# Optimization experiments

Measured on AMD Instinct MI355X. Metric: run time of the kernel, lower is better.

The kernel has to match this reference:

```python
import jax, jax.numpy as jnp
import numpy as np

# Detect() defaults from the source
NUM_CLASSES = 2
TOP_K = 750          # max detections returned per class
NMS_TOP_K = 5000     # candidates considered by NMS
NMS_THRESH = 0.3
CONF_THRESH = 0.05
VAR0, VAR1 = 0.1, 0.2  # prior box variances


def decode(loc, priors):
    # loc, priors: [P,4]; priors in (cx,cy,w,h); returns corner boxes [P,4]
    xy = priors[:, :2] + loc[:, :2] * VAR0 * priors[:, 2:]
    wh = priors[:, 2:] * jnp.exp(loc[:, 2:] * VAR1)
    x1y1 = xy - wh * 0.5
    x2y2 = x1y1 + wh
    return jnp.concatenate([x1y1, x2y2], axis=1)


def nms_single(boxes, scores):
    # boxes [P,4], scores [P] -> kept rows [TOP_K,5] = (score, x1,y1,x2,y2)
    s = jnp.where(scores > CONF_THRESH, scores, -1.0)
    top_s, top_i = jax.lax.top_k(s, NMS_TOP_K)   # restrict to best nms_top_k candidates
    cb = boxes[top_i]                             # [K,4] candidate boxes
    area = (cb[:, 2] - cb[:, 0]) * (cb[:, 3] - cb[:, 1])
    ar = jnp.arange(NMS_TOP_K)

    def step(s_cur, _):
        i = jnp.argmax(s_cur)                     # highest-scoring unsuppressed box
        sc = s_cur[i]
        ok = sc > 0.0                             # any valid candidate left?
        b = cb[i]
        xx1 = jnp.maximum(cb[:, 0], b[0])
        yy1 = jnp.maximum(cb[:, 1], b[1])
        xx2 = jnp.minimum(cb[:, 2], b[2])
        yy2 = jnp.minimum(cb[:, 3], b[3])
        inter = jnp.clip(xx2 - xx1, 0.0) * jnp.clip(yy2 - yy1, 0.0)
        union = area - inter + area[i]
        iou = inter / union
        supp = (iou > NMS_THRESH) | (ar == i)     # suppress overlapping + self
        s_next = jnp.where(ok & supp, -1.0, s_cur)
        row = jnp.where(ok, jnp.concatenate([sc[None], b]), jnp.zeros(5, boxes.dtype))
        return s_next, row

    _, rows = jax.lax.scan(step, top_s, None, length=TOP_K)
    return rows  # [TOP_K, 5]


def setup_inputs() -> dict:
    key = jax.random.key(0)
    k1, k2, k3 = jax.random.split(key, 3)
    B, P = 8, 136500
    loc_data = jax.random.normal(k1, (B, P, 4), jnp.float32)
    conf_data = jax.random.normal(k2, (B, P, 2), jnp.float32)
    u = jax.random.uniform(k3, (P, 4), jnp.float32)
    # priors: cx,cy in (0,1); w,h small positive (normalized coords)
    prior_data = jnp.concatenate([u[:, :2], u[:, 2:] * 0.1 + 0.01], axis=1)
    return {"loc_data": loc_data, "conf_data": conf_data, "prior_data": prior_data}


def reference(loc_data, conf_data, prior_data):
    B = loc_data.shape[0]
    conf = jax.nn.softmax(conf_data, axis=-1)                    # [B,P,2]
    boxes = jax.vmap(lambda l: decode(l, prior_data))(loc_data)  # [B,P,4]
    rows = jax.vmap(nms_single)(boxes, conf[:, :, 1])            # [B,TOP_K,5]
    out = jnp.zeros((B, NUM_CLASSES, TOP_K, 5), loc_data.dtype)  # class 0 = background, all zeros
    out = out.at[:, 1].set(rows)
    return out
```

## Files before the change

### kernel.cpp

```cpp
#include <hip/hip_runtime.h>
#include <stdint.h>

#pragma clang fp contract(off)

#define NPRI   136500
#define BATCH  8
#define NMS_K  5000
#define NKPAD  5120
#define TOPK   750
#define SORT_N 8192
#define HBINS  1024
#define HOFF   0x3D40
#define MROW   80
#define CNTSTRIDE 32
#define CUT    32

typedef unsigned long long u64;

__device__ __forceinline__ u64 shfl64(u64 v, int src) {
    int lo = __shfl((int)(unsigned)(v & 0xffffffffull), src);
    int hi = __shfl((int)(unsigned)(v >> 32), src);
    return ((u64)(unsigned)hi << 32) | (u64)(unsigned)lo;
}
__device__ __forceinline__ u64 shfl64_xor(u64 v, int m) {
    int lo = __shfl_xor((int)(unsigned)(v & 0xffffffffull), m);
    int hi = __shfl_xor((int)(unsigned)(v >> 32), m);
    return ((u64)(unsigned)hi << 32) | (u64)(unsigned)lo;
}

__device__ __forceinline__ bool iou_sup(float4 c4, float aj,
                                        float4 rbx, float ra) {
    float xx1 = fmaxf(c4.x, rbx.x);
    float yy1 = fmaxf(c4.y, rbx.y);
    float xx2 = fminf(c4.z, rbx.z);
    float yy2 = fminf(c4.w, rbx.w);
    float iw = fmaxf(xx2 - xx1, 0.0f);
    float ih = fmaxf(yy2 - yy1, 0.0f);
    float inter = iw * ih;
    float uni = (aj - inter) + ra;
    float u = fmaf(-0.3f, uni, inter);
    float d = fmaf(-1.4901161193847656e-8f, uni, u);
    return d > 0.0f;
}
__device__ __forceinline__ u64 iou_word(float4 c4, float aj,
                                        float4 rbx, float ra) {
    return __ballot(iou_sup(c4, aj, rbx, ra));
}

__device__ __forceinline__ u64 diag_mask(u64 word, int sh) {
    if (sh >= 0)
        word &= (sh >= 63) ? 0ull : (~0ull << (sh + 1));
    return word;
}

__device__ u64 row_word_slow(const float4* __restrict__ cbp,
                             const float* __restrict__ cap,
                             float4 rbx, float ra, int W) {
    int jbase = W << 6;
    u64 word = 0ull;
    for (int jj = 0; jj < 64; ++jj) {
        int jc = min(jbase + jj, NMS_K - 1);
        if (iou_sup(cbp[jc], cap[jc], rbx, ra)) word |= (1ull << jj);
    }
    return word;
}

__global__ __launch_bounds__(256) void score_hist_kernel(
        const float* __restrict__ conf, unsigned int* __restrict__ hist,
        float* __restrict__ sraw) {
    int b = blockIdx.y;
    __shared__ unsigned int h[HBINS];
    for (int i = threadIdx.x; i < HBINS; i += 256) h[i] = 0;
    __syncthreads();
    for (int p = blockIdx.x * 256 + threadIdx.x; p < NPRI; p += 64 * 256) {
        float2 c = ((const float2*)conf)[(size_t)b * NPRI + p];
        float m  = fmaxf(c.x, c.y);
        float e0 = expf(c.x - m), e1 = expf(c.y - m);
        float s  = e1 / (e0 + e1);
        sraw[(size_t)b * NPRI + p] = s;
        if (s > 0.05f) {
            int bin = (int)(__float_as_uint(s) >> 16) - HOFF;
            bin = min(max(bin, 0), HBINS - 1);
            atomicAdd(&h[bin], 1u);
        }
    }
    __syncthreads();
    for (int i = threadIdx.x; i < HBINS; i += 256) {
        unsigned int v = h[i];
        if (v) atomicAdd(&hist[b * HBINS + i], v);
    }
}

__global__ __launch_bounds__(1024) void scan_kernel(
        const unsigned int* __restrict__ hist, int* __restrict__ tbin) {
    int b = blockIdx.x, t = threadIdx.x;
    __shared__ unsigned int v[HBINS];
    __shared__ int best;
    v[t] = hist[b * HBINS + t];
    if (t == 0) best = 0;
    __syncthreads();
    for (int o = 1; o < HBINS; o <<= 1) {
        unsigned int add = (t + o < HBINS) ? v[t + o] : 0u;
        __syncthreads();
        v[t] += add;
        __syncthreads();
    }
    if (v[t] >= (unsigned)NMS_K) atomicMax(&best, t);
    __syncthreads();
    if (t == 0) tbin[b] = best;
}

__global__ __launch_bounds__(256) void compact_kernel(
        const float* __restrict__ sraw, const int* __restrict__ tbin,
        u64* __restrict__ keys, unsigned int* __restrict__ cnt) {
    int b = blockIdx.y;
    int tid = threadIdx.x;
    int lane = tid & 63;
    __shared__ u64 buf[2304];
    __shared__ unsigned int nloc;
    __shared__ unsigned int base_sh;
    if (tid == 0) nloc = 0;
    __syncthreads();
    int tb = tbin[b];
    for (int p = blockIdx.x * 256 + tid; p < NPRI; p += 64 * 256) {
        float s = sraw[(size_t)b * NPRI + p];
        bool pass = false;
        unsigned int bits = 0;
        if (s > 0.05f) {
            bits = __float_as_uint(s);
            int bin = (int)(bits >> 16) - HOFF;
            bin = min(max(bin, 0), HBINS - 1);
            pass = (bin >= tb);
        }
        u64 bal = __ballot(pass);
        int rank = (int)__popcll(bal & ((1ull << lane) - 1ull));
        unsigned int wbase = 0;
        if (lane == 0 && bal)
            wbase = atomicAdd(&nloc, (unsigned)__popcll(bal));
        wbase = (unsigned)__shfl((int)wbase, 0);
        if (pass)
            buf[wbase + rank] = ((u64)bits << 32) | (u64)(~(unsigned int)p);
    }
    __syncthreads();
    unsigned int tot = nloc;
    if (tid == 0)
        base_sh = tot ? atomicAdd(&cnt[b * CNTSTRIDE], tot) : 0u;
    __syncthreads();
    unsigned int base = base_sh;
    for (unsigned int i = tid; i < tot; i += 256) {
        unsigned int pos = base + i;
        if (pos < SORT_N)
            keys[(size_t)b * SORT_N + pos] = buf[i];
    }
}

__global__ __launch_bounds__(256) void sort1k_kernel(
        u64* __restrict__ keys, const unsigned int* __restrict__ cnt) {
    int b = blockIdx.y, c = blockIdx.x;
    int tid = threadIdx.x;
    int n = min((int)cnt[b * CNTSTRIDE], SORT_N);
    int base = c * 1024;
    if (base >= n) {
        for (int i = tid; i < 1024; i += 256)
            keys[(size_t)b * SORT_N + base + i] = 0ull;
        return;
    }
    __shared__ u64 k[1024];
    for (int i = tid; i < 1024; i += 256)
        k[i] = (base + i < n) ? keys[(size_t)b * SORT_N + base + i] : 0ull;
    __syncthreads();
    for (int kk = 2; kk <= 1024; kk <<= 1) {
        bool top = (kk == 1024);
        for (int j = kk >> 1; j > 0; j >>= 1) {
            for (int i = tid; i < 1024; i += 256) {
                int ixj = i ^ j;
                if (ixj > i) {
                    u64 a = k[i], v = k[ixj];
                    bool desc = top || ((i & kk) == 0);
                    if (desc ? (a < v) : (a > v)) { k[i] = v; k[ixj] = a; }
                }
            }
            __syncthreads();
        }
    }
    for (int i = tid; i < 1024; i += 256)
        keys[(size_t)b * SORT_N + base + i] = k[i];
}

__global__ __launch_bounds__(256) void merge0_kernel(
        const u64* __restrict__ keys, u64* __restrict__ keys2) {
    int b = blockIdx.y;
    int o = blockIdx.x * 256 + threadIdx.x;
    int pair = o >> 11;
    int oo = o & 2047;
    const u64* A  = keys + (size_t)b * SORT_N + pair * 2048;
    const u64* Bp = A + 1024;
    int lo = max(0, oo - 1024), hi = min(oo, 1024);
    while (lo < hi) {
        int mid = (lo + hi + 1) >> 1;
        bool ok = (oo - mid >= 1024) || (A[mid - 1] >= Bp[oo - mid]);
        if (ok) lo = mid; else hi = mid - 1;
    }
    int i = lo, j = oo - lo;
    u64 v;
    if (j >= 1024) v = A[i];
    else if (i >= 1024) v = Bp[j];
    else v = (A[i] >= Bp[j]) ? A[i] : Bp[j];
    keys2[(size_t)b * SORT_N + pair * 2048 + oo] = v;
}

__global__ __launch_bounds__(256) void merge1_kernel(
        const u64* __restrict__ keys2, u64* __restrict__ keys) {
    int b = blockIdx.y;
    int o = blockIdx.x * 256 + threadIdx.x;
    int pair = o >> 12;
    int oo = o & 4095;
    const u64* A  = keys2 + (size_t)b * SORT_N + pair * 4096;
    const u64* Bp = A + 2048;
    int lo = max(0, oo - 2048), hi = min(oo, 2048);
    while (lo < hi) {
        int mid = (lo + hi + 1) >> 1;
        bool ok = (oo - mid >= 2048) || (A[mid - 1] >= Bp[oo - mid]);
        if (ok) lo = mid; else hi = mid - 1;
    }
    int i = lo, j = oo - lo;
    u64 v;
    if (j >= 2048) v = A[i];
    else if (i >= 2048) v = Bp[j];
    else v = (A[i] >= Bp[j]) ? A[i] : Bp[j];
    keys[(size_t)b * SORT_N + pair * 4096 + oo] = v;
}

__global__ __launch_bounds__(256) void merge2_decode_kernel(
        const u64* __restrict__ keys,
        const float* __restrict__ loc, const float* __restrict__ priors,
        float* __restrict__ cscore, float* __restrict__ cbox,
        float* __restrict__ carea) {
    int b = blockIdx.y;
    int o = blockIdx.x * 256 + threadIdx.x;
    const u64* A  = keys + (size_t)b * SORT_N;
    const u64* Bp = A + 4096;
    int lo = max(0, o - 4096), hi = min(o, 4096);
    while (lo < hi) {
        int mid = (lo + hi + 1) >> 1;
        bool ok = (o - mid >= 4096) || (A[mid - 1] >= Bp[o - mid]);
        if (ok) lo = mid; else hi = mid - 1;
    }
    int i = lo, j = o - lo;
    u64 key;
    if (j >= 4096) key = A[i];
    else if (i >= 4096) key = Bp[j];
    else key = (A[i] >= Bp[j]) ? A[i] : Bp[j];
    if (o >= NMS_K) return;
    float sc; int idx;
    if (key != 0ull) {
        sc  = __uint_as_float((unsigned int)(key >> 32));
        idx = (int)(~(unsigned int)key);
    } else { sc = -1.0f; idx = 0; }
    cscore[b * NMS_K + o] = sc;
    float x1 = 0.f, y1 = 0.f, x2 = 0.f, y2 = 0.f, ar = 0.f;
    if (key != 0ull) {
        const float* l  = loc + ((size_t)b * NPRI + idx) * 4;
        const float* pr = priors + (size_t)idx * 4;
        float lx = l[0], ly = l[1], lw = l[2], lh = l[3];
        float pcx = pr[0], pcy = pr[1], pw = pr[2], ph = pr[3];
        float cx = pcx + (lx * 0.1f) * pw;
        float cy = pcy + (ly * 0.1f) * ph;
        float wd = pw * expf(lw * 0.2f);
        float ht = ph * expf(lh * 0.2f);
        x1 = cx - wd * 0.5f;  y1 = cy - ht * 0.5f;
        x2 = x1 + wd;         y2 = y1 + ht;
        ar = (x2 - x1) * (y2 - y1);
    }
    float* cb = cbox + ((size_t)b * NMS_K + o) * 4;
    cb[0] = x1; cb[1] = y1; cb[2] = x2; cb[3] = y2;
    carea[b * NMS_K + o] = ar;
}

__global__ __launch_bounds__(256, 4) void maskbuild_kernel(
        const float* __restrict__ cbox, const float* __restrict__ carea,
        u64* __restrict__ M) {
    int b   = blockIdx.y;
    int bid = blockIdx.x;
    int wgq, rb;
    if (bid >= 380) { wgq = 19; rb = bid - 380; }
    else {
        int w = (int)((sqrtf((float)(4 * bid + 5)) - 1.0f) * 0.5f);
        while (w * (w + 1) > bid) w--;
        while ((w + 1) * (w + 2) <= bid) w++;
        wgq = w; rb = bid - w * (w + 1);
    }
    int tid  = threadIdx.x;
    int lane = tid & 63;
    int wv   = __builtin_amdgcn_readfirstlane(tid >> 6);
    int w0   = wgq * 4;
    int rowbase = rb * 128;

    __shared__ float4 rbox[128];
    __shared__ float  rarea[128];
    if (tid < 128) {
        int i  = rowbase + tid;
        int ic = min(i, NMS_K - 1);
        rbox[tid]  = ((const float4*)cbox)[(size_t)b * NMS_K + ic];
        rarea[tid] = carea[(size_t)b * NMS_K + ic];
    }
    const float4* __restrict__ cbp = (const float4*)cbox + (size_t)b * NMS_K;
    const float*  __restrict__ cap = carea + (size_t)b * NMS_K;
    int j0 = w0 * 64 + lane;
    float4 c4_0 = cbp[min(j0,       NMS_K - 1)];
    float4 c4_1 = cbp[min(j0 +  64, NMS_K - 1)];
    float4 c4_2 = cbp[min(j0 + 128, NMS_K - 1)];
    float4 c4_3 = cbp[min(j0 + 192, NMS_K - 1)];
    float aj0 = cap[min(j0,       NMS_K - 1)];
    float aj1 = cap[min(j0 +  64, NMS_K - 1)];
    float aj2 = cap[min(j0 + 128, NMS_K - 1)];
    float aj3 = cap[min(j0 + 192, NMS_K - 1)];
    __syncthreads();

    int lr0 = 32 * wv;
    int rglob0 = rowbase + lr0;
    if (rglob0 >= NMS_K) return;

    u64* __restrict__ Mb = M + (size_t)b * NKPAD * MROW;

    if (rglob0 + 31 < w0 * 64) {
#pragma unroll 2
        for (int q = 0; q < 32; q += 2) {
            int lr = lr0 + q;
            float4 rb0 = rbox[lr], rb1 = rbox[lr + 1];
            float  ra0 = rarea[lr], ra1 = rarea[lr + 1];
            u64 A0 = iou_word(c4_0, aj0, rb0, ra0);
            u64 B0 = iou_word(c4_0, aj0, rb1, ra1);
            u64 A1 = iou_word(c4_1, aj1, rb0, ra0);
            u64 B1 = iou_word(c4_1, aj1, rb1, ra1);
            u64 A2 = iou_word(c4_2, aj2, rb0, ra0);
            u64 B2 = iou_word(c4_2, aj2, rb1, ra1);
            u64 A3 = iou_word(c4_3, aj3, rb0, ra0);
            u64 B3 = iou_word(c4_3, aj3, rb1, ra1);
            int row0 = rglob0 + q;
            if (lane == 0) {
                u64* d0 = Mb + (size_t)row0 * MROW + w0;
                ((ulonglong2*)d0)[0] = make_ulonglong2(A0, A1);
                ((ulonglong2*)d0)[1] = make_ulonglong2(A2, A3);
                u64* d1 = d0 + MROW;
                ((ulonglong2*)d1)[0] = make_ulonglong2(B0, B1);
                ((ulonglong2*)d1)[1] = make_ulonglong2(B2, B3);
            }
        }
    } else {
        int nrows = min(32, NMS_K - rglob0);
        int sh_base = rglob0 - w0 * 64;
#pragma unroll 2
        for (int q = 0; q < nrows; q += 2) {
            int lr = lr0 + q;
            float4 rb0 = rbox[lr], rb1 = rbox[lr + 1];
            float  ra0 = rarea[lr], ra1 = rarea[lr + 1];
            u64 A0 = iou_word(c4_0, aj0, rb0, ra0);
            u64 B0 = iou_word(c4_0, aj0, rb1, ra1);
            u64 A1 = iou_word(c4_1, aj1, rb0, ra0);
            u64 B1 = iou_word(c4_1, aj1, rb1, ra1);
            u64 A2 = iou_word(c4_2, aj2, rb0, ra0);
            u64 B2 = iou_word(c4_2, aj2, rb1, ra1);
            u64 A3 = iou_word(c4_3, aj3, rb0, ra0);
            u64 B3 = iou_word(c4_3, aj3, rb1, ra1);
            int sh = sh_base + q;
            A0 = diag_mask(A0, sh);       B0 = diag_mask(B0, sh + 1);
            A1 = diag_mask(A1, sh - 64);  B1 = diag_mask(B1, sh - 63);
            A2 = diag_mask(A2, sh - 128); B2 = diag_mask(B2, sh - 127);
            A3 = diag_mask(A3, sh - 192); B3 = diag_mask(B3, sh - 191);
            int row0 = rglob0 + q;
            if (lane == 0) {
                u64* d0 = Mb + (size_t)row0 * MROW + w0;
                ((ulonglong2*)d0)[0] = make_ulonglong2(A0, A1);
                ((ulonglong2*)d0)[1] = make_ulonglong2(A2, A3);
                u64* d1 = d0 + MROW;
                ((ulonglong2*)d1)[0] = make_ulonglong2(B0, B1);
                ((ulonglong2*)d1)[1] = make_ulonglong2(B2, B3);
            }
        }
    }
}

__global__ __launch_bounds__(1024) void maskscan_kernel(
        const float* __restrict__ cscore, const float* __restrict__ cbox,
        const float* __restrict__ carea,
        const unsigned int* __restrict__ cnt, const u64* __restrict__ M,
        float* __restrict__ out) {
    int b = blockIdx.x;
    int tid = threadIdx.x, lane = tid & 63, wv = tid >> 6;
    int nv = min((int)cnt[b * CNTSTRIDE], NMS_K);
    const u64* MB = M + (size_t)b * NKPAD * MROW;
    const float4* __restrict__ cbp = (const float4*)cbox + (size_t)b * NMS_K;
    const float*  __restrict__ cap = carea + (size_t)b * NMS_K;
    float* outb = out + (size_t)b * 2 * TOPK * 5;
    __shared__ unsigned int supp4[4];
    __shared__ u64 dbuf[2][64];
    __shared__ short allp[TOPK];
    __shared__ int emitted_sh;
    for (int i = tid; i < 2 * TOPK * 5; i += 1024) outb[i] = 0.f;
    if (tid < 4) supp4[tid] = 0u;
    if (tid == 0) emitted_sh = 0;
    if (wv == 1) dbuf[0][lane] = MB[(size_t)lane * MROW];
    __syncthreads();
    int emitted = 0;
    int nwords = (nv + 63) >> 6;
    u64 colw_prev = 0ull;
    u64 pickprev  = 0ull;
    for (int w = 0; w < nwords; w++) {
        int par = w & 1;
        if (wv == 0) {
            u64 colw;
            if (w + 1 < CUT) {
                colw = MB[(size_t)(w * 64 + lane) * MROW + (w + 1)];
            } else {
                int rc = min(w * 64 + lane, NMS_K - 1);
                colw = row_word_slow(cbp, cap, cbp[rc], cap[rc], w + 1);
            }
            u64 D = dbuf[par][lane];
            u64 sup = ((u64)supp4[2 * par + 1] << 32) | (u64)supp4[2 * par];
            if (lane == 0) {
                supp4[2 * par] = 0u;
                supp4[2 * par + 1] = 0u;
            }
            u64 x = ((pickprev >> lane) & 1ull) ? colw_prev : 0ull;
#pragma unroll
            for (int m = 1; m < 64; m <<= 1) x |= shfl64_xor(x, m);
            sup |= x;
            int base = w * 64, rem = nv - base;
            u64 valid = (rem >= 64) ? ~0ull : ((1ull << rem) - 1ull);
            u64 alive = valid & ~sup;
            u64 nz = __ballot(D != 0ull);
            u64 pickmask = 0ull;
            while (alive) {
                u64 blockers = alive & nz;
                if (!blockers) { pickmask |= alive; break; }
                int nb = __builtin_ctzll(blockers);
                u64 mle = (nb >= 63) ? ~0ull : ((1ull << (nb + 1)) - 1ull);
                pickmask |= alive & mle;
                u64 rw = shfl64(D, nb);
                alive &= ~mle;
                alive &= ~rw;
            }
            int room = TOPK - emitted;
            int pc = __popcll(pickmask);
            while (pc > room) {
                pickmask &= ~(1ull << (63 - __builtin_clzll(pickmask)));
                pc--;
            }
            if (lane == 0) emitted_sh = emitted + pc;
            if ((pickmask >> lane) & 1ull) {
                int rank = (int)__popcll(pickmask & ((1ull << lane) - 1ull));
                allp[emitted + rank] = (short)(base + lane);
            }
            pickprev = pickmask;
            colw_prev = colw;
        } else if (wv == 1) {
            if (w + 1 < nwords) {
                int W = w + 1;
                u64 dpre;
                if (W < CUT) {
                    dpre = MB[(size_t)(W * 64 + lane) * MROW + W];
                } else {
                    int rc = min(W * 64 + lane, NMS_K - 1);
                    dpre = diag_mask(
                        row_word_slow(cbp, cap, cbp[rc], cap[rc], W), lane);
                }
                dbuf[W & 1][lane] = dpre;
            }
        } else {
            int i = (wv - 2) * 64 + lane;
            u64 v = 0ull;
            if (i < emitted) {
                int pr = allp[i];
                if (w + 1 < CUT)
                    v = MB[(size_t)pr * MROW + (w + 1)];
                else
                    v = row_word_slow(cbp, cap, cbp[pr], cap[pr], w + 1);
            }
#pragma unroll
            for (int m = 1; m < 64; m <<= 1) v |= shfl64_xor(v, m);
            if (lane == 0 && v) {
                atomicOr(&supp4[2 * (par ^ 1)],     (unsigned int)v);
                atomicOr(&supp4[2 * (par ^ 1) + 1], (unsigned int)(v >> 32));
            }
        }
        __syncthreads();
        emitted = emitted_sh;
        if (emitted >= TOPK) break;
    }
    for (int t = tid; t < emitted; t += 1024) {
        int p = allp[t];
        float sc  = cscore[b * NMS_K + p];
        float4 bx = ((const float4*)cbox)[(size_t)b * NMS_K + p];
        float* o = outb + (size_t)(TOPK + t) * 5;
        o[0] = sc; o[1] = bx.x; o[2] = bx.y; o[3] = bx.z; o[4] = bx.w;
    }
}

extern "C" void kernel_launch(void* const* d_in, const int* in_sizes, int n_in,
                              void* d_out, int out_size, void* d_ws, size_t ws_size,
                              hipStream_t stream) {
    const float* loc    = (const float*)d_in[0];
    const float* conf   = (const float*)d_in[1];
    const float* priors = (const float*)d_in[2];
    float* out = (float*)d_out;

    char* ws = (char*)d_ws;
    size_t off = 0;
    unsigned int* hist = (unsigned int*)(ws + off);   off += (size_t)BATCH * HBINS * 4;
    unsigned int* cnt  = (unsigned int*)(ws + off);   off += (size_t)BATCH * CNTSTRIDE * 4;
    size_t zero_bytes = off;
    int* tbin = (int*)(ws + off);                     off += 256;
    u64* keys  = (u64*)(ws + off);                    off += (size_t)BATCH * SORT_N * 8;
    u64* keys2 = (u64*)(ws + off);                    off += (size_t)BATCH * SORT_N * 8;
    float* cscore = (float*)(ws + off);               off += (size_t)BATCH * NMS_K * 4;
    float* cbox   = (float*)(ws + off);               off += (size_t)BATCH * NMS_K * 16;
    float* carea  = (float*)(ws + off);               off += (size_t)BATCH * NMS_K * 4;
    u64* M = (u64*)(ws + off);                        off += (size_t)BATCH * NKPAD * MROW * 8;
    float* sraw = (float*)M;

    hipMemsetAsync(d_ws, 0, zero_bytes, stream);

    score_hist_kernel<<<dim3(64, BATCH), 256, 0, stream>>>(conf, hist, sraw);
    scan_kernel<<<BATCH, HBINS, 0, stream>>>(hist, tbin);
    compact_kernel<<<dim3(64, BATCH), 256, 0, stream>>>(sraw, tbin, keys, cnt);
    sort1k_kernel<<<dim3(8, BATCH), 256, 0, stream>>>(keys, cnt);
    merge0_kernel<<<dim3(32, BATCH), 256, 0, stream>>>(keys, keys2);
    merge1_kernel<<<dim3(32, BATCH), 256, 0, stream>>>(keys2, keys);
    merge2_decode_kernel<<<dim3(20, BATCH), 256, 0, stream>>>(keys, loc, priors, cscore, cbox, carea);
    maskbuild_kernel<<<dim3(72, BATCH), 256, 0, stream>>>(cbox, carea, M);
    maskscan_kernel<<<BATCH, 1024, 0, stream>>>(cscore, cbox, carea, cnt, M, out);
}
```

Measured before the change: 183.0 us.

## Fuse chunk sort, merge passes and decode into one per-batch LDS bitonic sort

```diff
diff --git a/kernel.cpp b/kernel.cpp
--- a/kernel.cpp
+++ b/kernel.cpp
@@ -154,25 +154,22 @@
     }
 }
 
-__global__ __launch_bounds__(256) void sort1k_kernel(
-        u64* __restrict__ keys, const unsigned int* __restrict__ cnt) {
-    int b = blockIdx.y, c = blockIdx.x;
+__global__ __launch_bounds__(1024) void sortdecode_kernel(
+        u64* __restrict__ keys, const unsigned int* __restrict__ cnt,
+        const float* __restrict__ loc, const float* __restrict__ priors,
+        float* __restrict__ cscore, float* __restrict__ cbox,
+        float* __restrict__ carea) {
+    int b = blockIdx.x;
     int tid = threadIdx.x;
+    __shared__ u64 k[SORT_N];
     int n = min((int)cnt[b * CNTSTRIDE], SORT_N);
-    int base = c * 1024;
-    if (base >= n) {
-        for (int i = tid; i < 1024; i += 256)
-            keys[(size_t)b * SORT_N + base + i] = 0ull;
-        return;
-    }
-    __shared__ u64 k[1024];
-    for (int i = tid; i < 1024; i += 256)
-        k[i] = (base + i < n) ? keys[(size_t)b * SORT_N + base + i] : 0ull;
-    __syncthreads();
-    for (int kk = 2; kk <= 1024; kk <<= 1) {
-        bool top = (kk == 1024);
+    for (int i = tid; i < SORT_N; i += 1024)
+        k[i] = (i < n) ? keys[(size_t)b * SORT_N + i] : 0ull;
+    __syncthreads();
+    for (int kk = 2; kk <= SORT_N; kk <<= 1) {
+        bool top = (kk == SORT_N);
         for (int j = kk >> 1; j > 0; j >>= 1) {
-            for (int i = tid; i < 1024; i += 256) {
+            for (int i = tid; i < SORT_N; i += 1024) {
                 int ixj = i ^ j;
                 if (ixj > i) {
                     u64 a = k[i], v = k[ixj];
@@ -183,98 +180,32 @@
             __syncthreads();
         }
     }
-    for (int i = tid; i < 1024; i += 256)
-        keys[(size_t)b * SORT_N + base + i] = k[i];
-}
-
-__global__ __launch_bounds__(256) void merge0_kernel(
-        const u64* __restrict__ keys, u64* __restrict__ keys2) {
-    int b = blockIdx.y;
-    int o = blockIdx.x * 256 + threadIdx.x;
-    int pair = o >> 11;
-    int oo = o & 2047;
-    const u64* A  = keys + (size_t)b * SORT_N + pair * 2048;
-    const u64* Bp = A + 1024;
-    int lo = max(0, oo - 1024), hi = min(oo, 1024);
-    while (lo < hi) {
-        int mid = (lo + hi + 1) >> 1;
-        bool ok = (oo - mid >= 1024) || (A[mid - 1] >= Bp[oo - mid]);
-        if (ok) lo = mid; else hi = mid - 1;
-    }
-    int i = lo, j = oo - lo;
-    u64 v;
-    if (j >= 1024) v = A[i];
-    else if (i >= 1024) v = Bp[j];
-    else v = (A[i] >= Bp[j]) ? A[i] : Bp[j];
-    keys2[(size_t)b * SORT_N + pair * 2048 + oo] = v;
-}
-
-__global__ __launch_bounds__(256) void merge1_kernel(
-        const u64* __restrict__ keys2, u64* __restrict__ keys) {
-    int b = blockIdx.y;
-    int o = blockIdx.x * 256 + threadIdx.x;
-    int pair = o >> 12;
-    int oo = o & 4095;
-    const u64* A  = keys2 + (size_t)b * SORT_N + pair * 4096;
-    const u64* Bp = A + 2048;
-    int lo = max(0, oo - 2048), hi = min(oo, 2048);
-    while (lo < hi) {
-        int mid = (lo + hi + 1) >> 1;
-        bool ok = (oo - mid >= 2048) || (A[mid - 1] >= Bp[oo - mid]);
-        if (ok) lo = mid; else hi = mid - 1;
-    }
-    int i = lo, j = oo - lo;
-    u64 v;
-    if (j >= 2048) v = A[i];
-    else if (i >= 2048) v = Bp[j];
-    else v = (A[i] >= Bp[j]) ? A[i] : Bp[j];
-    keys[(size_t)b * SORT_N + pair * 4096 + oo] = v;
-}
-
-__global__ __launch_bounds__(256) void merge2_decode_kernel(
-        const u64* __restrict__ keys,
-        const float* __restrict__ loc, const float* __restrict__ priors,
-        float* __restrict__ cscore, float* __restrict__ cbox,
-        float* __restrict__ carea) {
-    int b = blockIdx.y;
-    int o = blockIdx.x * 256 + threadIdx.x;
-    const u64* A  = keys + (size_t)b * SORT_N;
-    const u64* Bp = A + 4096;
-    int lo = max(0, o - 4096), hi = min(o, 4096);
-    while (lo < hi) {
-        int mid = (lo + hi + 1) >> 1;
-        bool ok = (o - mid >= 4096) || (A[mid - 1] >= Bp[o - mid]);
-        if (ok) lo = mid; else hi = mid - 1;
-    }
-    int i = lo, j = o - lo;
-    u64 key;
-    if (j >= 4096) key = A[i];
-    else if (i >= 4096) key = Bp[j];
-    else key = (A[i] >= Bp[j]) ? A[i] : Bp[j];
-    if (o >= NMS_K) return;
-    float sc; int idx;
-    if (key != 0ull) {
-        sc  = __uint_as_float((unsigned int)(key >> 32));
-        idx = (int)(~(unsigned int)key);
-    } else { sc = -1.0f; idx = 0; }
-    cscore[b * NMS_K + o] = sc;
-    float x1 = 0.f, y1 = 0.f, x2 = 0.f, y2 = 0.f, ar = 0.f;
-    if (key != 0ull) {
-        const float* l  = loc + ((size_t)b * NPRI + idx) * 4;
-        const float* pr = priors + (size_t)idx * 4;
-        float lx = l[0], ly = l[1], lw = l[2], lh = l[3];
-        float pcx = pr[0], pcy = pr[1], pw = pr[2], ph = pr[3];
-        float cx = pcx + (lx * 0.1f) * pw;
-        float cy = pcy + (ly * 0.1f) * ph;
-        float wd = pw * expf(lw * 0.2f);
-        float ht = ph * expf(lh * 0.2f);
-        x1 = cx - wd * 0.5f;  y1 = cy - ht * 0.5f;
-        x2 = x1 + wd;         y2 = y1 + ht;
-        ar = (x2 - x1) * (y2 - y1);
-    }
-    float* cb = cbox + ((size_t)b * NMS_K + o) * 4;
-    cb[0] = x1; cb[1] = y1; cb[2] = x2; cb[3] = y2;
-    carea[b * NMS_K + o] = ar;
+    for (int o = tid; o < NMS_K; o += 1024) {
+        u64 key = k[o];
+        float sc; int idx;
+        if (key != 0ull) {
+            sc  = __uint_as_float((unsigned int)(key >> 32));
+            idx = (int)(~(unsigned int)key);
+        } else { sc = -1.0f; idx = 0; }
+        cscore[b * NMS_K + o] = sc;
+        float x1 = 0.f, y1 = 0.f, x2 = 0.f, y2 = 0.f, ar = 0.f;
+        if (key != 0ull) {
+            const float* l  = loc + ((size_t)b * NPRI + idx) * 4;
+            const float* pr = priors + (size_t)idx * 4;
+            float lx = l[0], ly = l[1], lw = l[2], lh = l[3];
+            float pcx = pr[0], pcy = pr[1], pw = pr[2], ph = pr[3];
+            float cx = pcx + (lx * 0.1f) * pw;
+            float cy = pcy + (ly * 0.1f) * ph;
+            float wd = pw * expf(lw * 0.2f);
+            float ht = ph * expf(lh * 0.2f);
+            x1 = cx - wd * 0.5f;  y1 = cy - ht * 0.5f;
+            x2 = x1 + wd;         y2 = y1 + ht;
+            ar = (x2 - x1) * (y2 - y1);
+        }
+        float* cb = cbox + ((size_t)b * NMS_K + o) * 4;
+        cb[0] = x1; cb[1] = y1; cb[2] = x2; cb[3] = y2;
+        carea[b * NMS_K + o] = ar;
+    }
 }
 
 __global__ __launch_bounds__(256, 4) void maskbuild_kernel(
@@ -512,7 +443,6 @@
     size_t zero_bytes = off;
     int* tbin = (int*)(ws + off);                     off += 256;
     u64* keys  = (u64*)(ws + off);                    off += (size_t)BATCH * SORT_N * 8;
-    u64* keys2 = (u64*)(ws + off);                    off += (size_t)BATCH * SORT_N * 8;
     float* cscore = (float*)(ws + off);               off += (size_t)BATCH * NMS_K * 4;
     float* cbox   = (float*)(ws + off);               off += (size_t)BATCH * NMS_K * 16;
     float* carea  = (float*)(ws + off);               off += (size_t)BATCH * NMS_K * 4;
@@ -524,10 +454,7 @@
     score_hist_kernel<<<dim3(64, BATCH), 256, 0, stream>>>(conf, hist, sraw);
     scan_kernel<<<BATCH, HBINS, 0, stream>>>(hist, tbin);
     compact_kernel<<<dim3(64, BATCH), 256, 0, stream>>>(sraw, tbin, keys, cnt);
-    sort1k_kernel<<<dim3(8, BATCH), 256, 0, stream>>>(keys, cnt);
-    merge0_kernel<<<dim3(32, BATCH), 256, 0, stream>>>(keys, keys2);
-    merge1_kernel<<<dim3(32, BATCH), 256, 0, stream>>>(keys2, keys);
-    merge2_decode_kernel<<<dim3(20, BATCH), 256, 0, stream>>>(keys, loc, priors, cscore, cbox, carea);
+    sortdecode_kernel<<<BATCH, 1024, 0, stream>>>(keys, cnt, loc, priors, cscore, cbox, carea);
     maskbuild_kernel<<<dim3(72, BATCH), 256, 0, stream>>>(cbox, carea, M);
     maskscan_kernel<<<BATCH, 1024, 0, stream>>>(cscore, cbox, carea, cnt, M, out);
 }
```

Result: slower. 273.8 us (+49.6%).
